# Kernel tuning notes

Measured on AMD Instinct MI355X. Metric: run time of the kernel, lower is better.

## Reference

```python
import jax, jax.numpy as jnp
import numpy as np

RADIUS = 50.0
EPS = 1e-8


def setup_inputs() -> dict:
    key = jax.random.key(0)
    k1, k2, k3, k4, k5 = jax.random.split(key, 5)
    N, E, H = 16384, 524288, 256
    x = jax.random.normal(k1, (N, H), dtype=jnp.float32)
    edge_index = jax.random.randint(k2, (2, E), 0, N, dtype=jnp.int32)
    spatial_coords = jax.random.uniform(k3, (N, 2), dtype=jnp.float32) * 1000.0
    w1 = jax.random.normal(k4, (3, H // 2), dtype=jnp.float32) * 0.02
    b1 = jnp.zeros((H // 2,), dtype=jnp.float32)
    w2 = jax.random.normal(k5, (H // 2, H), dtype=jnp.float32) * 0.02
    b2 = jnp.zeros((H,), dtype=jnp.float32)
    return {"x": x, "edge_index": edge_index, "spatial_coords": spatial_coords,
            "w1": w1, "b1": b1, "w2": w2, "b2": b2}


def reference(x, edge_index, spatial_coords, w1, b1, w2, b2):
    N = x.shape[0]
    row, col = edge_index[0], edge_index[1]

    # degree via scatter-add (segment_sum)
    ones = jnp.ones(row.shape, dtype=x.dtype)
    degree = jax.ops.segment_sum(ones, row, num_segments=N)  # [N]

    # spatial density: count neighbors within RADIUS (full pairwise, vectorized)
    sq = jnp.sum(spatial_coords * spatial_coords, axis=-1)  # [N]
    d2 = sq[:, None] + sq[None, :] - 2.0 * (spatial_coords @ spatial_coords.T)  # [N,N] squared dists
    in_radius = (d2 <= RADIUS * RADIUS).astype(x.dtype)
    density = jnp.sum(in_radius, axis=1) - 1.0  # exclude self
    density = density / (jnp.max(density) + EPS)

    # local feature variance: || x - mean(neighbor features) ||
    nbr_sum = jax.ops.segment_sum(x[col], row, num_segments=N)  # [N,H]
    cnt = jnp.clip(degree, 1.0)[:, None]
    nbr_mean = nbr_sum / cnt
    fvar = jnp.linalg.norm(x - nbr_mean, axis=-1)  # [N]
    fvar = fvar / (jnp.max(fvar) + EPS)

    feats = jnp.stack([degree / (jnp.max(degree) + EPS), density, fvar], axis=-1)  # [N,3]
    h = jax.nn.relu(feats @ w1 + b1)
    return h @ w2 + b2  # [N, hidden_dim]
```

## Files before the change

### kernel.cpp

```cpp
#include <hip/hip_runtime.h>
#include <math.h>

#define R2 2500.0f
#define EPSF 1e-8f

constexpr int H   = 256;
constexpr int HH  = 128;
constexpr int NB  = 8;
constexpr int BSH = 11;
constexpr int RPW = 2;

__global__ void __launch_bounds__(256) k_degcell(
    const int* __restrict__ row, const int* __restrict__ col,
    int* __restrict__ deg4, const float* __restrict__ coords,
    int* __restrict__ cellcnt, int E, int EB, int N) {
    if ((int)blockIdx.x < EB) {
        int e = blockIdx.x * 256 + threadIdx.x;
        if (e < E) atomicAdd(&deg4[row[e] * NB + (col[e] >> BSH)], 1);
    } else {
        int t = ((int)blockIdx.x - EB) * 256 + threadIdx.x;
        if (t < N) {
            float2 c = ((const float2*)coords)[t];
            int cx = (int)(c.x * 0.02f); if (cx > 19) cx = 19;
            int cy = (int)(c.y * 0.02f); if (cy > 19) cy = 19;
            atomicAdd(&cellcnt[cy * 20 + cx], 1);
        }
    }
}

__global__ void __launch_bounds__(256) k_bsum(const int* __restrict__ deg4,
                                              int* __restrict__ bsum) {
    int t = threadIdx.x;
    int4 v = ((const int4*)deg4)[blockIdx.x * 256 + t];
    int sum = v.x + v.y + v.z + v.w;
#pragma unroll
    for (int off = 32; off > 0; off >>= 1) sum += __shfl_xor(sum, off, 64);
    __shared__ int sw[4];
    if ((t & 63) == 0) sw[t >> 6] = sum;
    __syncthreads();
    if (t == 0) bsum[blockIdx.x] = sw[0] + sw[1] + sw[2] + sw[3];
}

__global__ void __launch_bounds__(512) k_scatcell(
    const int* __restrict__ deg4, const int* __restrict__ bsum,
    int* __restrict__ rp4, int* __restrict__ cur4, int M,
    const int* __restrict__ cellcnt, int* __restrict__ cellstart,
    int* __restrict__ cellcur) {
    __shared__ int s[512];
    int t = threadIdx.x;
    int blk = blockIdx.x;
    if (blk < gridDim.x - 1) {
        s[t] = (t < 128) ? bsum[t] : 0;
        __syncthreads();
        for (int off = 1; off < 128; off <<= 1) {
            int v = (t < 128) ? s[t] : 0;
            int add = (t >= off && t < 128) ? s[t - off] : 0;
            __syncthreads();
            if (t < 128) s[t] = v + add;
            __syncthreads();
        }
        int boff = (blk > 0) ? s[blk - 1] : 0;
        if (t < 256) {
            int lane = t & 63, w = t >> 6;
            int4 v = ((const int4*)deg4)[blk * 256 + t];
            int tsum = v.x + v.y + v.z + v.w;
            int incl = tsum;
#pragma unroll
            for (int off = 1; off < 64; off <<= 1) {
                int n = __shfl_up(incl, off, 64);
                if (lane >= off) incl += n;
            }
            __shared__ int wsum[4];
            if (lane == 63) wsum[w] = incl;
            __syncthreads();
            int woff = 0;
#pragma unroll
            for (int k = 0; k < 4; k++) woff += (k < w) ? wsum[k] : 0;
            int excl = boff + woff + (incl - tsum);
            int4 r;
            r.x = excl;
            r.y = excl + v.x;
            r.z = excl + v.x + v.y;
            r.w = excl + v.x + v.y + v.z;
            ((int4*)rp4)[blk * 256 + t]  = r;
            ((int4*)cur4)[blk * 256 + t] = r;
            if (blk == 127 && t == 255) rp4[M] = excl + tsum;
        }
    } else {
        s[t] = (t < 400) ? cellcnt[t] : 0;
        __syncthreads();
        for (int off = 1; off < 512; off <<= 1) {
            int v = s[t];
            int add = (t >= off) ? s[t - off] : 0;
            __syncthreads();
            s[t] = v + add;
            __syncthreads();
        }
        if (t < 400) {
            int excl = (t > 0) ? s[t - 1] : 0;
            cellstart[t] = excl;
            cellcur[t]   = excl;
        }
        if (t == 400) cellstart[400] = s[399];
    }
}

__global__ void __launch_bounds__(256) k_fillcell(
    const int* __restrict__ row, const int* __restrict__ col,
    int* __restrict__ cur4, int* __restrict__ cols,
    const float* __restrict__ coords, int* __restrict__ cellcur,
    float4* __restrict__ pts, int E, int EB, int N) {
    if ((int)blockIdx.x < EB) {
        int e = blockIdx.x * 256 + threadIdx.x;
        if (e < E) {
            int r = row[e], c = col[e];
            int p = atomicAdd(&cur4[r * NB + (c >> BSH)], 1);
            cols[p] = c;
        }
    } else {
        int t = ((int)blockIdx.x - EB) * 256 + threadIdx.x;
        if (t < N) {
            float2 c = ((const float2*)coords)[t];
            int cx = (int)(c.x * 0.02f); if (cx > 19) cx = 19;
            int cy = (int)(c.y * 0.02f); if (cy > 19) cy = 19;
            int p = atomicAdd(&cellcur[cy * 20 + cx], 1);
            pts[p] = make_float4(c.x, c.y, c.x * c.x + c.y * c.y, __int_as_float(t));
        }
    }
}

__global__ void __launch_bounds__(256) k_dgrid(
    const float4* __restrict__ pts, const int* __restrict__ cellstart,
    int* __restrict__ dens, int N) {
    int wave = threadIdx.x >> 6;
    int lane = threadIdx.x & 63;
    int t = blockIdx.x * 4 + wave;
    float4 p = pts[t];
    int cx = (int)(p.x * 0.02f); if (cx > 19) cx = 19;
    int cy = (int)(p.y * 0.02f); if (cy > 19) cy = 19;
    int x0 = cx - 2; if (x0 < 0) x0 = 0;
    int x1 = cx + 2; if (x1 > 19) x1 = 19;
    int y0 = cy - 2; if (y0 < 0) y0 = 0;
    int y1 = cy + 2; if (y1 > 19) y1 = 19;
    int cnt = 0;
    for (int yy = y0; yy <= y1; yy++) {
        int rowb = yy * 20;
        int s = cellstart[rowb + x0];
        int e = cellstart[rowb + x1 + 1];
        for (int q = s + lane; q < e; q += 64) {
            float4 pq = pts[q];
            float dot = p.x * pq.x + p.y * pq.y;
            float d2 = (p.z + pq.z) - 2.0f * dot;
            cnt += (d2 <= R2) ? 1 : 0;
        }
    }
#pragma unroll
    for (int off = 32; off > 0; off >>= 1) cnt += __shfl_xor(cnt, off, 64);
    if (lane == 0) dens[__float_as_int(p.w)] = cnt;
}

__global__ void __launch_bounds__(256, 8) k_fvar(
    const float* __restrict__ x, const int* __restrict__ rp4,
    const int* __restrict__ cols, float* __restrict__ fvar, int N) {
    int wave = threadIdx.x >> 6;
    int lane = threadIdx.x & 63;
    int i0 = (blockIdx.x * 4 + wave) * RPW;
    const float4* xb = (const float4*)x;

    int bnd = rp4[i0 * NB + (lane < 2 * NB ? lane : 2 * NB)];

    float4 acc0 = make_float4(0.f, 0.f, 0.f, 0.f);
    float4 acc1 = make_float4(0.f, 0.f, 0.f, 0.f);

    for (int b = 0; b < NB; b++) {
#pragma unroll
        for (int r = 0; r < RPW; r++) {
            float4& a = (r == 0) ? acc0 : acc1;
            int s = __shfl(bnd, r * NB + b, 64);
            int e = __shfl(bnd, r * NB + b + 1, 64);
            if (e <= s) continue;
            for (int p0 = s; p0 < e; p0 += 64) {
                int m = e - p0; if (m > 64) m = 64;
                int idx = cols[p0 + (lane < m ? lane : m - 1)];
                for (int j = 0; j < m; j += 8) {
                    int nb2 = m - j; if (nb2 > 8) nb2 = 8;
                    size_t o0 = (size_t)__shfl(idx, j + 0, 64) * 64 + lane;
                    size_t o1 = (1 < nb2) ? (size_t)__shfl(idx, j + 1, 64) * 64 + lane : 0;
                    size_t o2 = (2 < nb2) ? (size_t)__shfl(idx, j + 2, 64) * 64 + lane : 0;
                    size_t o3 = (3 < nb2) ? (size_t)__shfl(idx, j + 3, 64) * 64 + lane : 0;
                    size_t o4 = (4 < nb2) ? (size_t)__shfl(idx, j + 4, 64) * 64 + lane : 0;
                    size_t o5 = (5 < nb2) ? (size_t)__shfl(idx, j + 5, 64) * 64 + lane : 0;
                    size_t o6 = (6 < nb2) ? (size_t)__shfl(idx, j + 6, 64) * 64 + lane : 0;
                    size_t o7 = (7 < nb2) ? (size_t)__shfl(idx, j + 7, 64) * 64 + lane : 0;
                    float4 g0 = xb[o0];
                    float4 g1 = xb[o1];
                    float4 g2 = xb[o2];
                    float4 g3 = xb[o3];
                    float4 g4 = xb[o4];
                    float4 g5 = xb[o5];
                    float4 g6 = xb[o6];
                    float4 g7 = xb[o7];
                    float w1 = (1 < nb2) ? 1.0f : 0.0f;
                    float w2 = (2 < nb2) ? 1.0f : 0.0f;
                    float w3 = (3 < nb2) ? 1.0f : 0.0f;
                    float w4 = (4 < nb2) ? 1.0f : 0.0f;
                    float w5 = (5 < nb2) ? 1.0f : 0.0f;
                    float w6 = (6 < nb2) ? 1.0f : 0.0f;
                    float w7 = (7 < nb2) ? 1.0f : 0.0f;
                    a.x += g0.x; a.y += g0.y; a.z += g0.z; a.w += g0.w;
                    a.x = fmaf(g1.x, w1, a.x); a.y = fmaf(g1.y, w1, a.y);
                    a.z = fmaf(g1.z, w1, a.z); a.w = fmaf(g1.w, w1, a.w);
                    a.x = fmaf(g2.x, w2, a.x); a.y = fmaf(g2.y, w2, a.y);
                    a.z = fmaf(g2.z, w2, a.z); a.w = fmaf(g2.w, w2, a.w);
                    a.x = fmaf(g3.x, w3, a.x); a.y = fmaf(g3.y, w3, a.y);
                    a.z = fmaf(g3.z, w3, a.z); a.w = fmaf(g3.w, w3, a.w);
                    a.x = fmaf(g4.x, w4, a.x); a.y = fmaf(g4.y, w4, a.y);
                    a.z = fmaf(g4.z, w4, a.z); a.w = fmaf(g4.w, w4, a.w);
                    a.x = fmaf(g5.x, w5, a.x); a.y = fmaf(g5.y, w5, a.y);
                    a.z = fmaf(g5.z, w5, a.z); a.w = fmaf(g5.w, w5, a.w);
                    a.x = fmaf(g6.x, w6, a.x); a.y = fmaf(g6.y, w6, a.y);
                    a.z = fmaf(g6.z, w6, a.z); a.w = fmaf(g6.w, w6, a.w);
                    a.x = fmaf(g7.x, w7, a.x); a.y = fmaf(g7.y, w7, a.y);
                    a.z = fmaf(g7.z, w7, a.z); a.w = fmaf(g7.w, w7, a.w);
                }
            }
        }
    }

#define FIN(RR, ACCR)                                                   \
    {                                                                   \
        int i = i0 + (RR);                                              \
        float cnt = fmaxf((float)(__shfl(bnd, (RR) * NB + NB, 64) -     \
                                  __shfl(bnd, (RR) * NB, 64)), 1.0f);   \
        float4 xi = xb[(size_t)i * 64 + lane];                          \
        float dx = xi.x - ACCR.x / cnt;                                 \
        float dy = xi.y - ACCR.y / cnt;                                 \
        float dz = xi.z - ACCR.z / cnt;                                 \
        float dw = xi.w - ACCR.w / cnt;                                 \
        float ss = dx * dx + dy * dy + dz * dz + dw * dw;               \
        _Pragma("unroll")                                               \
        for (int off = 32; off > 0; off >>= 1) ss += __shfl_xor(ss, off, 64); \
        if (lane == 0) fvar[i] = sqrtf(ss);                             \
    }

    FIN(0, acc0);
    FIN(1, acc1);
#undef FIN
}

__global__ void __launch_bounds__(256) k_scal(
    const int* __restrict__ rp4, const int* __restrict__ dens,
    const float* __restrict__ fvar, int* __restrict__ scal, int N) {
    __shared__ int sd[4], sn[4];
    __shared__ float sf[4];
    int t = threadIdx.x;
    int g = blockIdx.x * 256 + t;
    int stride = 256 * gridDim.x;
    int md = 0, mn = 0;
    float mf = 0.f;
    for (int i = g; i < N; i += stride) {
        md = max(md, rp4[(i + 1) * NB] - rp4[i * NB]);
        mn = max(mn, dens[i]);
        mf = fmaxf(mf, fvar[i]);
    }
#pragma unroll
    for (int off = 32; off > 0; off >>= 1) {
        md = max(md, __shfl_xor(md, off, 64));
        mn = max(mn, __shfl_xor(mn, off, 64));
        mf = fmaxf(mf, __shfl_xor(mf, off, 64));
    }
    int w = t >> 6, l = t & 63;
    if (l == 0) { sd[w] = md; sn[w] = mn; sf[w] = mf; }
    __syncthreads();
    if (t == 0) {
#pragma unroll
        for (int k = 1; k < 4; k++) {
            md = max(md, sd[k]);
            mn = max(mn, sn[k]);
            mf = fmaxf(mf, sf[k]);
        }
        atomicMax(&scal[0], md);
        atomicMax(&scal[1], mn);
        atomicMax(&scal[2], __float_as_int(mf));
    }
}

__global__ void __launch_bounds__(256) k_mlp(
    const float* __restrict__ w1, const float* __restrict__ b1,
    const float* __restrict__ w2, const float* __restrict__ b2,
    const int* __restrict__ rp4, const int* __restrict__ dens,
    const float* __restrict__ fvar, const int* __restrict__ scal,
    float* __restrict__ out, int N) {
    __shared__ float sh_h[HH];
    int j = threadIdx.x;
    float wv[HH];
#pragma unroll
    for (int l = 0; l < HH; l++) wv[l] = w2[l * H + j];
    float bj = b2[j];
    float maxdeg  = (float)scal[0] + EPSF;
    float maxdens = (float)(scal[1] - 1) + EPSF;
    float maxfv   = __int_as_float(scal[2]) + EPSF;
    float w1a = 0.f, w1b = 0.f, w1c = 0.f, b1j = 0.f;
    if (j < HH) { w1a = w1[j]; w1b = w1[HH + j]; w1c = w1[2 * HH + j]; b1j = b1[j]; }
    for (int i = blockIdx.x; i < N; i += gridDim.x) {
        float f0 = (float)(rp4[(i + 1) * NB] - rp4[i * NB]) / maxdeg;
        float f1 = (float)(dens[i] - 1) / maxdens;
        float f2 = fvar[i] / maxfv;
        if (j < HH) {
            float h = f0 * w1a + f1 * w1b + f2 * w1c + b1j;
            sh_h[j] = fmaxf(h, 0.0f);
        }
        __syncthreads();
        float acc = bj;
#pragma unroll
        for (int l = 0; l < HH; l++) acc = fmaf(sh_h[l], wv[l], acc);
        out[(size_t)i * H + j] = acc;
        __syncthreads();
    }
}

extern "C" void kernel_launch(void* const* d_in, const int* in_sizes, int n_in,
                              void* d_out, int out_size, void* d_ws, size_t ws_size,
                              hipStream_t stream) {
    const float* x      = (const float*)d_in[0];
    const int*   ei     = (const int*)d_in[1];
    const float* coords = (const float*)d_in[2];
    const float* w1     = (const float*)d_in[3];
    const float* b1     = (const float*)d_in[4];
    const float* w2     = (const float*)d_in[5];
    const float* b2     = (const float*)d_in[6];
    float* out = (float*)d_out;

    const int N = in_sizes[2] / 2;
    const int E = in_sizes[1] / 2;
    const int M = N * NB;
    const int NBLK = M / 1024;
    const int EB = (E + 255) / 256;
    const int CB = N / 256;
    const int* row = ei;
    const int* col = ei + E;

    int* ws        = (int*)d_ws;
    int* scal      = ws;
    int* deg4      = ws + 4;
    int* cellcnt   = ws + 4 + M;
    int* rp4       = ws + 408 + M;
    int* cur4      = rp4 + M + 4;
    int* cellstart = cur4 + M;
    int* cellcur   = cellstart + 404;
    int* dens_cnt  = cellcur + 400;
    float* fvarp   = (float*)(dens_cnt + N);
    int* bsum      = dens_cnt + 2 * N;
    int* boff      = bsum + 128;
    int* cols      = boff + 128;
    float4* pts    = (float4*)(cols + E);

    hipMemsetAsync(ws, 0, (size_t)(408 + M) * sizeof(int), stream);

    k_degcell<<<EB + CB, 256, 0, stream>>>(row, col, deg4, coords, cellcnt, E, EB, N);
    k_bsum<<<NBLK, 256, 0, stream>>>(deg4, bsum);
    k_scatcell<<<NBLK + 1, 512, 0, stream>>>(deg4, bsum, rp4, cur4, M,
                                             cellcnt, cellstart, cellcur);
    k_fillcell<<<EB + CB, 256, 0, stream>>>(row, col, cur4, cols,
                                            coords, cellcur, pts, E, EB, N);

    k_dgrid<<<N / 4, 256, 0, stream>>>(pts, cellstart, dens_cnt, N);

    k_fvar<<<N / (4 * RPW), 256, 0, stream>>>(x, rp4, cols, fvarp, N);

    k_scal<<<64, 256, 0, stream>>>(rp4, dens_cnt, fvarp, scal, N);

    k_mlp<<<1024, 256, 0, stream>>>(w1, b1, w2, b2, rp4, dens_cnt, fvarp, scal,
                                    out, N);
}
```

Baseline: 253.7 us.

## Fuse density grid and feature-variance kernels; vectorize edge atomics; raise rows per wave

```diff
diff --git a/kernel.cpp b/kernel.cpp
--- a/kernel.cpp
+++ b/kernel.cpp
@@ -8,23 +8,29 @@
 constexpr int HH  = 128;
 constexpr int NB  = 8;
 constexpr int BSH = 11;
-constexpr int RPW = 2;
+constexpr int RPW = 4;
 
 __global__ void __launch_bounds__(256) k_degcell(
     const int* __restrict__ row, const int* __restrict__ col,
     int* __restrict__ deg4, const float* __restrict__ coords,
-    int* __restrict__ cellcnt, int E, int EB, int N) {
-    if ((int)blockIdx.x < EB) {
-        int e = blockIdx.x * 256 + threadIdx.x;
-        if (e < E) atomicAdd(&deg4[row[e] * NB + (col[e] >> BSH)], 1);
+    int* __restrict__ cellcnt, int EB4, int N) {
+    if ((int)blockIdx.x < EB4) {
+        int e4 = blockIdx.x * 256 + threadIdx.x;
+        int4 r = ((const int4*)row)[e4];
+        int4 c = ((const int4*)col)[e4];
+        atomicAdd(&deg4[r.x * NB + (c.x >> BSH)], 1);
+        atomicAdd(&deg4[r.y * NB + (c.y >> BSH)], 1);
+        atomicAdd(&deg4[r.z * NB + (c.z >> BSH)], 1);
+        atomicAdd(&deg4[r.w * NB + (c.w >> BSH)], 1);
     } else {
-        int t = ((int)blockIdx.x - EB) * 256 + threadIdx.x;
-        if (t < N) {
-            float2 c = ((const float2*)coords)[t];
-            int cx = (int)(c.x * 0.02f); if (cx > 19) cx = 19;
-            int cy = (int)(c.y * 0.02f); if (cy > 19) cy = 19;
-            atomicAdd(&cellcnt[cy * 20 + cx], 1);
-        }
+        int t2 = ((int)blockIdx.x - EB4) * 256 + threadIdx.x;
+        float4 cc = ((const float4*)coords)[t2];
+        int cx0 = (int)(cc.x * 0.02f); if (cx0 > 19) cx0 = 19;
+        int cy0 = (int)(cc.y * 0.02f); if (cy0 > 19) cy0 = 19;
+        int cx1 = (int)(cc.z * 0.02f); if (cx1 > 19) cx1 = 19;
+        int cy1 = (int)(cc.w * 0.02f); if (cy1 > 19) cy1 = 19;
+        atomicAdd(&cellcnt[cy0 * 20 + cx0], 1);
+        atomicAdd(&cellcnt[cy1 * 20 + cx1], 1);
     }
 }
 
@@ -109,143 +115,152 @@
     const int* __restrict__ row, const int* __restrict__ col,
     int* __restrict__ cur4, int* __restrict__ cols,
     const float* __restrict__ coords, int* __restrict__ cellcur,
-    float4* __restrict__ pts, int E, int EB, int N) {
-    if ((int)blockIdx.x < EB) {
-        int e = blockIdx.x * 256 + threadIdx.x;
-        if (e < E) {
-            int r = row[e], c = col[e];
-            int p = atomicAdd(&cur4[r * NB + (c >> BSH)], 1);
-            cols[p] = c;
-        }
+    float4* __restrict__ pts, int EB4, int N) {
+    if ((int)blockIdx.x < EB4) {
+        int e4 = blockIdx.x * 256 + threadIdx.x;
+        int4 r = ((const int4*)row)[e4];
+        int4 c = ((const int4*)col)[e4];
+        int p0 = atomicAdd(&cur4[r.x * NB + (c.x >> BSH)], 1); cols[p0] = c.x;
+        int p1 = atomicAdd(&cur4[r.y * NB + (c.y >> BSH)], 1); cols[p1] = c.y;
+        int p2 = atomicAdd(&cur4[r.z * NB + (c.z >> BSH)], 1); cols[p2] = c.z;
+        int p3 = atomicAdd(&cur4[r.w * NB + (c.w >> BSH)], 1); cols[p3] = c.w;
     } else {
-        int t = ((int)blockIdx.x - EB) * 256 + threadIdx.x;
-        if (t < N) {
-            float2 c = ((const float2*)coords)[t];
-            int cx = (int)(c.x * 0.02f); if (cx > 19) cx = 19;
-            int cy = (int)(c.y * 0.02f); if (cy > 19) cy = 19;
-            int p = atomicAdd(&cellcur[cy * 20 + cx], 1);
-            pts[p] = make_float4(c.x, c.y, c.x * c.x + c.y * c.y, __int_as_float(t));
-        }
-    }
-}
-
-__global__ void __launch_bounds__(256) k_dgrid(
+        int t2 = ((int)blockIdx.x - EB4) * 256 + threadIdx.x;
+        float4 cc = ((const float4*)coords)[t2];
+        int i0 = t2 * 2;
+        int cx0 = (int)(cc.x * 0.02f); if (cx0 > 19) cx0 = 19;
+        int cy0 = (int)(cc.y * 0.02f); if (cy0 > 19) cy0 = 19;
+        int p0 = atomicAdd(&cellcur[cy0 * 20 + cx0], 1);
+        pts[p0] = make_float4(cc.x, cc.y, cc.x * cc.x + cc.y * cc.y,
+                              __int_as_float(i0));
+        int cx1 = (int)(cc.z * 0.02f); if (cx1 > 19) cx1 = 19;
+        int cy1 = (int)(cc.w * 0.02f); if (cy1 > 19) cy1 = 19;
+        int p1 = atomicAdd(&cellcur[cy1 * 20 + cx1], 1);
+        pts[p1] = make_float4(cc.z, cc.w, cc.z * cc.z + cc.w * cc.w,
+                              __int_as_float(i0 + 1));
+    }
+}
+
+__global__ void __launch_bounds__(256, 8) k_fvar_dgrid(
+    const float* __restrict__ x, const int* __restrict__ rp4,
+    const int* __restrict__ cols, float* __restrict__ fvar,
     const float4* __restrict__ pts, const int* __restrict__ cellstart,
-    int* __restrict__ dens, int N) {
+    int* __restrict__ dens, int FBk, int N) {
     int wave = threadIdx.x >> 6;
     int lane = threadIdx.x & 63;
-    int t = blockIdx.x * 4 + wave;
-    float4 p = pts[t];
-    int cx = (int)(p.x * 0.02f); if (cx > 19) cx = 19;
-    int cy = (int)(p.y * 0.02f); if (cy > 19) cy = 19;
-    int x0 = cx - 2; if (x0 < 0) x0 = 0;
-    int x1 = cx + 2; if (x1 > 19) x1 = 19;
-    int y0 = cy - 2; if (y0 < 0) y0 = 0;
-    int y1 = cy + 2; if (y1 > 19) y1 = 19;
-    int cnt = 0;
-    for (int yy = y0; yy <= y1; yy++) {
-        int rowb = yy * 20;
-        int s = cellstart[rowb + x0];
-        int e = cellstart[rowb + x1 + 1];
-        for (int q = s + lane; q < e; q += 64) {
-            float4 pq = pts[q];
-            float dot = p.x * pq.x + p.y * pq.y;
-            float d2 = (p.z + pq.z) - 2.0f * dot;
-            cnt += (d2 <= R2) ? 1 : 0;
-        }
-    }
-#pragma unroll
-    for (int off = 32; off > 0; off >>= 1) cnt += __shfl_xor(cnt, off, 64);
-    if (lane == 0) dens[__float_as_int(p.w)] = cnt;
-}
-
-__global__ void __launch_bounds__(256, 8) k_fvar(
-    const float* __restrict__ x, const int* __restrict__ rp4,
-    const int* __restrict__ cols, float* __restrict__ fvar, int N) {
-    int wave = threadIdx.x >> 6;
-    int lane = threadIdx.x & 63;
-    int i0 = (blockIdx.x * 4 + wave) * RPW;
-    const float4* xb = (const float4*)x;
-
-    int bnd = rp4[i0 * NB + (lane < 2 * NB ? lane : 2 * NB)];
-
-    float4 acc0 = make_float4(0.f, 0.f, 0.f, 0.f);
-    float4 acc1 = make_float4(0.f, 0.f, 0.f, 0.f);
-
-    for (int b = 0; b < NB; b++) {
-#pragma unroll
-        for (int r = 0; r < RPW; r++) {
-            float4& a = (r == 0) ? acc0 : acc1;
-            int s = __shfl(bnd, r * NB + b, 64);
-            int e = __shfl(bnd, r * NB + b + 1, 64);
-            if (e <= s) continue;
-            for (int p0 = s; p0 < e; p0 += 64) {
-                int m = e - p0; if (m > 64) m = 64;
-                int idx = cols[p0 + (lane < m ? lane : m - 1)];
-                for (int j = 0; j < m; j += 8) {
-                    int nb2 = m - j; if (nb2 > 8) nb2 = 8;
-                    size_t o0 = (size_t)__shfl(idx, j + 0, 64) * 64 + lane;
-                    size_t o1 = (1 < nb2) ? (size_t)__shfl(idx, j + 1, 64) * 64 + lane : 0;
-                    size_t o2 = (2 < nb2) ? (size_t)__shfl(idx, j + 2, 64) * 64 + lane : 0;
-                    size_t o3 = (3 < nb2) ? (size_t)__shfl(idx, j + 3, 64) * 64 + lane : 0;
-                    size_t o4 = (4 < nb2) ? (size_t)__shfl(idx, j + 4, 64) * 64 + lane : 0;
-                    size_t o5 = (5 < nb2) ? (size_t)__shfl(idx, j + 5, 64) * 64 + lane : 0;
-                    size_t o6 = (6 < nb2) ? (size_t)__shfl(idx, j + 6, 64) * 64 + lane : 0;
-                    size_t o7 = (7 < nb2) ? (size_t)__shfl(idx, j + 7, 64) * 64 + lane : 0;
-                    float4 g0 = xb[o0];
-                    float4 g1 = xb[o1];
-                    float4 g2 = xb[o2];
-                    float4 g3 = xb[o3];
-                    float4 g4 = xb[o4];
-                    float4 g5 = xb[o5];
-                    float4 g6 = xb[o6];
-                    float4 g7 = xb[o7];
-                    float w1 = (1 < nb2) ? 1.0f : 0.0f;
-                    float w2 = (2 < nb2) ? 1.0f : 0.0f;
-                    float w3 = (3 < nb2) ? 1.0f : 0.0f;
-                    float w4 = (4 < nb2) ? 1.0f : 0.0f;
-                    float w5 = (5 < nb2) ? 1.0f : 0.0f;
-                    float w6 = (6 < nb2) ? 1.0f : 0.0f;
-                    float w7 = (7 < nb2) ? 1.0f : 0.0f;
-                    a.x += g0.x; a.y += g0.y; a.z += g0.z; a.w += g0.w;
-                    a.x = fmaf(g1.x, w1, a.x); a.y = fmaf(g1.y, w1, a.y);
-                    a.z = fmaf(g1.z, w1, a.z); a.w = fmaf(g1.w, w1, a.w);
-                    a.x = fmaf(g2.x, w2, a.x); a.y = fmaf(g2.y, w2, a.y);
-                    a.z = fmaf(g2.z, w2, a.z); a.w = fmaf(g2.w, w2, a.w);
-                    a.x = fmaf(g3.x, w3, a.x); a.y = fmaf(g3.y, w3, a.y);
-                    a.z = fmaf(g3.z, w3, a.z); a.w = fmaf(g3.w, w3, a.w);
-                    a.x = fmaf(g4.x, w4, a.x); a.y = fmaf(g4.y, w4, a.y);
-                    a.z = fmaf(g4.z, w4, a.z); a.w = fmaf(g4.w, w4, a.w);
-                    a.x = fmaf(g5.x, w5, a.x); a.y = fmaf(g5.y, w5, a.y);
-                    a.z = fmaf(g5.z, w5, a.z); a.w = fmaf(g5.w, w5, a.w);
-                    a.x = fmaf(g6.x, w6, a.x); a.y = fmaf(g6.y, w6, a.y);
-                    a.z = fmaf(g6.z, w6, a.z); a.w = fmaf(g6.w, w6, a.w);
-                    a.x = fmaf(g7.x, w7, a.x); a.y = fmaf(g7.y, w7, a.y);
-                    a.z = fmaf(g7.z, w7, a.z); a.w = fmaf(g7.w, w7, a.w);
+    if ((int)blockIdx.x < FBk) {
+        int i0 = (blockIdx.x * 4 + wave) * RPW;
+        const float4* xb = (const float4*)x;
+
+        int bnd = rp4[i0 * NB + (lane < 4 * NB ? lane : 4 * NB)];
+
+        float4 acc0 = make_float4(0.f, 0.f, 0.f, 0.f);
+        float4 acc1 = make_float4(0.f, 0.f, 0.f, 0.f);
+        float4 acc2 = make_float4(0.f, 0.f, 0.f, 0.f);
+        float4 acc3 = make_float4(0.f, 0.f, 0.f, 0.f);
+
+        for (int b = 0; b < NB; b++) {
+#pragma unroll
+            for (int r = 0; r < RPW; r++) {
+                float4& a = (r == 0) ? acc0 : (r == 1) ? acc1
+                          : (r == 2) ? acc2 : acc3;
+                int s = __shfl(bnd, r * NB + b, 64);
+                int e = __shfl(bnd, r * NB + b + 1, 64);
+                if (e <= s) continue;
+                for (int p0 = s; p0 < e; p0 += 64) {
+                    int m = e - p0; if (m > 64) m = 64;
+                    int idx = cols[p0 + (lane < m ? lane : m - 1)];
+                    for (int j = 0; j < m; j += 8) {
+                        int nb2 = m - j; if (nb2 > 8) nb2 = 8;
+                        size_t o0 = (size_t)__shfl(idx, j + 0, 64) * 64 + lane;
+                        size_t o1 = (1 < nb2) ? (size_t)__shfl(idx, j + 1, 64) * 64 + lane : 0;
+                        size_t o2 = (2 < nb2) ? (size_t)__shfl(idx, j + 2, 64) * 64 + lane : 0;
+                        size_t o3 = (3 < nb2) ? (size_t)__shfl(idx, j + 3, 64) * 64 + lane : 0;
+                        size_t o4 = (4 < nb2) ? (size_t)__shfl(idx, j + 4, 64) * 64 + lane : 0;
+                        size_t o5 = (5 < nb2) ? (size_t)__shfl(idx, j + 5, 64) * 64 + lane : 0;
+                        size_t o6 = (6 < nb2) ? (size_t)__shfl(idx, j + 6, 64) * 64 + lane : 0;
+                        size_t o7 = (7 < nb2) ? (size_t)__shfl(idx, j + 7, 64) * 64 + lane : 0;
+                        float4 g0 = xb[o0];
+                        float4 g1 = xb[o1];
+                        float4 g2 = xb[o2];
+                        float4 g3 = xb[o3];
+                        float4 g4 = xb[o4];
+                        float4 g5 = xb[o5];
+                        float4 g6 = xb[o6];
+                        float4 g7 = xb[o7];
+                        float w1 = (1 < nb2) ? 1.0f : 0.0f;
+                        float w2 = (2 < nb2) ? 1.0f : 0.0f;
+                        float w3 = (3 < nb2) ? 1.0f : 0.0f;
+                        float w4 = (4 < nb2) ? 1.0f : 0.0f;
+                        float w5 = (5 < nb2) ? 1.0f : 0.0f;
+                        float w6 = (6 < nb2) ? 1.0f : 0.0f;
+                        float w7 = (7 < nb2) ? 1.0f : 0.0f;
+                        a.x += g0.x; a.y += g0.y; a.z += g0.z; a.w += g0.w;
+                        a.x = fmaf(g1.x, w1, a.x); a.y = fmaf(g1.y, w1, a.y);
+                        a.z = fmaf(g1.z, w1, a.z); a.w = fmaf(g1.w, w1, a.w);
+                        a.x = fmaf(g2.x, w2, a.x); a.y = fmaf(g2.y, w2, a.y);
+                        a.z = fmaf(g2.z, w2, a.z); a.w = fmaf(g2.w, w2, a.w);
+                        a.x = fmaf(g3.x, w3, a.x); a.y = fmaf(g3.y, w3, a.y);
+                        a.z = fmaf(g3.z, w3, a.z); a.w = fmaf(g3.w, w3, a.w);
+                        a.x = fmaf(g4.x, w4, a.x); a.y = fmaf(g4.y, w4, a.y);
+                        a.z = fmaf(g4.z, w4, a.z); a.w = fmaf(g4.w, w4, a.w);
+                        a.x = fmaf(g5.x, w5, a.x); a.y = fmaf(g5.y, w5, a.y);
+                        a.z = fmaf(g5.z, w5, a.z); a.w = fmaf(g5.w, w5, a.w);
+                        a.x = fmaf(g6.x, w6, a.x); a.y = fmaf(g6.y, w6, a.y);
+                        a.z = fmaf(g6.z, w6, a.z); a.w = fmaf(g6.w, w6, a.w);
+                        a.x = fmaf(g7.x, w7, a.x); a.y = fmaf(g7.y, w7, a.y);
+                        a.z = fmaf(g7.z, w7, a.z); a.w = fmaf(g7.w, w7, a.w);
+                    }
                 }
             }
         }
-    }
 
 #define FIN(RR, ACCR)                                                   \
-    {                                                                   \
-        int i = i0 + (RR);                                              \
-        float cnt = fmaxf((float)(__shfl(bnd, (RR) * NB + NB, 64) -     \
-                                  __shfl(bnd, (RR) * NB, 64)), 1.0f);   \
-        float4 xi = xb[(size_t)i * 64 + lane];                          \
-        float dx = xi.x - ACCR.x / cnt;                                 \
-        float dy = xi.y - ACCR.y / cnt;                                 \
-        float dz = xi.z - ACCR.z / cnt;                                 \
-        float dw = xi.w - ACCR.w / cnt;                                 \
-        float ss = dx * dx + dy * dy + dz * dz + dw * dw;               \
-        _Pragma("unroll")                                               \
-        for (int off = 32; off > 0; off >>= 1) ss += __shfl_xor(ss, off, 64); \
-        if (lane == 0) fvar[i] = sqrtf(ss);                             \
-    }
-
-    FIN(0, acc0);
-    FIN(1, acc1);
+        {                                                               \
+            int i = i0 + (RR);                                          \
+            float cnt = fmaxf((float)(__shfl(bnd, (RR) * NB + NB, 64) - \
+                                      __shfl(bnd, (RR) * NB, 64)), 1.0f); \
+            float4 xi = xb[(size_t)i * 64 + lane];                      \
+            float dx = xi.x - ACCR.x / cnt;                             \
+            float dy = xi.y - ACCR.y / cnt;                             \
+            float dz = xi.z - ACCR.z / cnt;                             \
+            float dw = xi.w - ACCR.w / cnt;                             \
+            float ss = dx * dx + dy * dy + dz * dz + dw * dw;           \
+            _Pragma("unroll")                                           \
+            for (int off = 32; off > 0; off >>= 1) ss += __shfl_xor(ss, off, 64); \
+            if (lane == 0) fvar[i] = sqrtf(ss);                         \
+        }
+
+        FIN(0, acc0);
+        FIN(1, acc1);
+        FIN(2, acc2);
+        FIN(3, acc3);
 #undef FIN
+    } else {
+        int t = ((int)blockIdx.x - FBk) * 4 + wave;
+        float4 p = pts[t];
+        int cx = (int)(p.x * 0.02f); if (cx > 19) cx = 19;
+        int cy = (int)(p.y * 0.02f); if (cy > 19) cy = 19;
+        int x0 = cx - 2; if (x0 < 0) x0 = 0;
+        int x1 = cx + 2; if (x1 > 19) x1 = 19;
+        int y0 = cy - 2; if (y0 < 0) y0 = 0;
+        int y1 = cy + 2; if (y1 > 19) y1 = 19;
+        int cnt = 0;
+        for (int yy = y0; yy <= y1; yy++) {
+            int rowb = yy * 20;
+            int s = cellstart[rowb + x0];
+            int e = cellstart[rowb + x1 + 1];
+            for (int q = s + lane; q < e; q += 64) {
+                float4 pq = pts[q];
+                float dot = p.x * pq.x + p.y * pq.y;
+                float d2 = (p.z + pq.z) - 2.0f * dot;
+                cnt += (d2 <= R2) ? 1 : 0;
+            }
+        }
+#pragma unroll
+        for (int off = 32; off > 0; off >>= 1) cnt += __shfl_xor(cnt, off, 64);
+        if (lane == 0) dens[__float_as_int(p.w)] = cnt;
+    }
 }
 
 __global__ void __launch_bounds__(256) k_scal(
@@ -335,8 +350,10 @@
     const int E = in_sizes[1] / 2;
     const int M = N * NB;
     const int NBLK = M / 1024;
-    const int EB = (E + 255) / 256;
-    const int CB = N / 256;
+    const int EB4 = E / 1024;
+    const int CB2 = N / 512;
+    const int FBk = N / (4 * RPW);
+    const int DB  = N / 4;
     const int* row = ei;
     const int* col = ei + E;
 
@@ -357,16 +374,16 @@
 
     hipMemsetAsync(ws, 0, (size_t)(408 + M) * sizeof(int), stream);
 
-    k_degcell<<<EB + CB, 256, 0, stream>>>(row, col, deg4, coords, cellcnt, E, EB, N);
+    k_degcell<<<EB4 + CB2, 256, 0, stream>>>(row, col, deg4, coords, cellcnt,
+                                             EB4, N);
     k_bsum<<<NBLK, 256, 0, stream>>>(deg4, bsum);
     k_scatcell<<<NBLK + 1, 512, 0, stream>>>(deg4, bsum, rp4, cur4, M,
                                              cellcnt, cellstart, cellcur);
-    k_fillcell<<<EB + CB, 256, 0, stream>>>(row, col, cur4, cols,
-                                            coords, cellcur, pts, E, EB, N);
-
-    k_dgrid<<<N / 4, 256, 0, stream>>>(pts, cellstart, dens_cnt, N);
-
-    k_fvar<<<N / (4 * RPW), 256, 0, stream>>>(x, rp4, cols, fvarp, N);
+    k_fillcell<<<EB4 + CB2, 256, 0, stream>>>(row, col, cur4, cols,
+                                              coords, cellcur, pts, EB4, N);
+
+    k_fvar_dgrid<<<FBk + DB, 256, 0, stream>>>(x, rp4, cols, fvarp,
+                                               pts, cellstart, dens_cnt, FBk, N);
 
     k_scal<<<64, 256, 0, stream>>>(rp4, dens_cnt, fvarp, scal, N);
 
```

After: 262.2 us. 3.4% more time.
